# Kernel tuning notes

Measured on AMD Instinct MI355X. Metric: run time of the kernel, lower is better.

## Reference

```python
import jax, jax.numpy as jnp
import numpy as np

SCALE = 0.125  # 1/sqrt(D_head=64)
NEG_INF = -1.0e9


def setup_inputs() -> dict:
    key = jax.random.key(0)
    kq, kk, kv, km = jax.random.split(key, 4)
    B, L, N, D = 2, 2048, 16, 64
    query = jax.random.normal(kq, (B, L, N, D), dtype=jnp.float32)
    k = jax.random.normal(kk, (B, L, N, D), dtype=jnp.float32)
    v = jax.random.normal(kv, (B, L, N, D), dtype=jnp.float32)
    attn_mask = jax.random.randint(km, (B, L, L), 0, 2).astype(jnp.bool_)
    return {"query": query, "key": k, "value": v, "attn_mask": attn_mask}


def reference(query, key, value, attn_mask):
    # scores: [B, L_q, L_k, N]
    attention = jnp.einsum('bind,bjnd->bijn', query, key) * SCALE
    # mask broadcast over heads; True positions are masked out
    attention = jnp.where(attn_mask[:, :, :, None], NEG_INF, attention)
    # softmax over the key axis (dim=2), dropout p=0.0 is identity
    attention = jax.nn.softmax(attention, axis=2)
    context = jnp.einsum('bijn,bjnd->bind', attention, value)
    return (context, attention)
```

## Files before the change

### kernel.cpp

```cpp
#include <hip/hip_runtime.h>
#include <hip/hip_bf16.h>

typedef unsigned short u16;
typedef unsigned char u8;
typedef __attribute__((ext_vector_type(8))) short bf16x8;
typedef __attribute__((ext_vector_type(4))) float f32x4;

#define MFMA16(a, b, c) __builtin_amdgcn_mfma_f32_16x16x32_bf16(a, b, c, 0, 0, 0)

#define LGKM_BARRIER()                                     \
    do {                                                   \
        asm volatile("s_waitcnt lgkmcnt(0)" ::: "memory"); \
        __builtin_amdgcn_s_barrier();                      \
        asm volatile("" ::: "memory");                     \
    } while (0)

static __device__ __forceinline__ u16 f2bf(float f) {
    __hip_bfloat16 h = __float2bfloat16(f);
    return *reinterpret_cast<u16*>(&h);
}
static __device__ __forceinline__ float bf2f(u16 h) {
    unsigned u = ((unsigned)h) << 16;
    return __uint_as_float(u);
}

__global__ __launch_bounds__(256) void kconv_kernel(const float* __restrict__ kf,
                                                    u16* __restrict__ kb) {
    const size_t i = ((size_t)blockIdx.x * 256 + threadIdx.x) * 4;
    float4 f = *(const float4*)(kf + i);
    alignas(8) u16 w[4] = {f2bf(f.x), f2bf(f.y), f2bf(f.z), f2bf(f.w)};
    *(uint2*)(kb + i) = *(const uint2*)w;
}

__global__ __launch_bounds__(256) void vt_kernel(const float* __restrict__ v,
                                                 u16* __restrict__ vt) {
    __shared__ u16 T[64][72];
    const int t = threadIdx.x, bid = blockIdx.x;
    const int b = bid >> 9, n = bid & 15, j0 = ((bid >> 4) & 31) << 6;
    {
        const int jj = t >> 4, tt = t & 15;
#pragma unroll
        for (int rep = 0; rep < 4; rep++) {
            const int j = rep * 16 + jj;
            const float* src = v + (((size_t)((b * 2048 + j0 + j) * 16 + n)) << 6) + tt * 4;
            float4 f = *(const float4*)src;
            alignas(8) u16 w[4] = {f2bf(f.x), f2bf(f.y), f2bf(f.z), f2bf(f.w)};
            *(uint2*)&T[j][tt * 4] = *(const uint2*)w;
        }
    }
    __syncthreads();
    {
        const int d = t >> 2, jq = t & 3;
        alignas(16) u16 w[16];
#pragma unroll
        for (int e = 0; e < 16; e++) w[e] = T[jq * 16 + e][d];
        u16* dst = vt + (((size_t)((b * 16 + n) * 64 + d)) << 11) + j0 + jq * 16;
        *(uint4*)dst = *(const uint4*)&w[0];
        *(uint4*)(dst + 8) = *(const uint4*)&w[8];
    }
}

#define LOADK(ra, rb, rc2, rd, jb)                            \
    do {                                                      \
        const int jw_ = (jb) & 2047;                          \
        const u16* kp0_ = kb + (size_t)(jw_ + c) * 1024;      \
        ra = *(const bf16x8*)kp0_;                            \
        rb = *(const bf16x8*)(kp0_ + 32);                     \
        const u16* kp1_ = kb + (size_t)(jw_ + 16 + c) * 1024; \
        rc2 = *(const bf16x8*)kp1_;                           \
        rd = *(const bf16x8*)(kp1_ + 32);                     \
    } while (0)

#define LOADV(r0, r1, r2, r3, jb)                             \
    do {                                                      \
        const int jw_ = (jb) & 2047;                          \
        const u16* vp_ = vb + (size_t)c * 2048 + jw_ + g * 8; \
        r0 = *(const bf16x8*)(vp_);                           \
        r1 = *(const bf16x8*)(vp_ + 16 * 2048);               \
        r2 = *(const bf16x8*)(vp_ + 32 * 2048);               \
        r3 = *(const bf16x8*)(vp_ + 48 * 2048);               \
    } while (0)

__global__ __launch_bounds__(1024, 4) void attn_kernel(
    const float* __restrict__ qf, const u16* __restrict__ kb_g,
    const u16* __restrict__ vt, const void* __restrict__ mask,
    float* __restrict__ ctx, float* __restrict__ attn) {
    __shared__ u16 maskT[2048];
    __shared__ u16 pbuf[2][16][16][40];

    const int tid = threadIdx.x;
    const int lane = tid & 63;
    const int wv = tid >> 6;
    const int g = lane >> 4, c = lane & 15;
    const int rbit = g * 4;

    const int bid = blockIdx.x;
    const int b = ((bid & 7) < 4) ? 0 : 1;
    const int idx = ((bid >> 3) << 2) | (bid & 3);
    const int i0 = idx << 4;

    bool mask_is_u8;
    {
        unsigned acc = 0;
        const unsigned* mw = (const unsigned*)mask;
#pragma unroll
        for (int i = 0; i < 64; i++) acc |= mw[i];
        mask_is_u8 = (acc & 0xFFFFFF00u) != 0u;
    }

    {
        const size_t base = ((size_t)(b * 2048 + i0)) * 2048 + (size_t)tid * 2;
        unsigned m0 = 0, m1 = 0;
        if (mask_is_u8) {
            const u8* m8 = (const u8*)mask;
#pragma unroll
            for (int i = 0; i < 16; i++) {
                const u8* mp = m8 + base + (size_t)i * 2048;
                if (mp[0]) m0 |= (1u << i);
                if (mp[1]) m1 |= (1u << i);
            }
        } else {
            const int* m32 = (const int*)mask;
#pragma unroll
            for (int i = 0; i < 16; i++) {
                const int* mp = m32 + base + (size_t)i * 2048;
                if (mp[0]) m0 |= (1u << i);
                if (mp[1]) m1 |= (1u << i);
            }
        }
        *reinterpret_cast<unsigned*>(&maskT[tid * 2]) = m0 | (m1 << 16);
    }
    __syncthreads();

    bf16x8 aq0, aq1;
    {
        const float* qp = qf + (((size_t)(b * 2048 + i0 + c) * 16 + wv) << 6) + g * 8;
        float4 f0 = *(const float4*)qp;
        float4 f1 = *(const float4*)(qp + 4);
        float4 f2 = *(const float4*)(qp + 32);
        float4 f3 = *(const float4*)(qp + 36);
        alignas(16) u16 w0[8] = {f2bf(f0.x), f2bf(f0.y), f2bf(f0.z), f2bf(f0.w),
                                 f2bf(f1.x), f2bf(f1.y), f2bf(f1.z), f2bf(f1.w)};
        alignas(16) u16 w1[8] = {f2bf(f2.x), f2bf(f2.y), f2bf(f2.z), f2bf(f2.w),
                                 f2bf(f3.x), f2bf(f3.y), f2bf(f3.z), f2bf(f3.w)};
        aq0 = *(const bf16x8*)w0;
        aq1 = *(const bf16x8*)w1;
    }

    const u16* kb = kb_g + (((size_t)(b * 2048) * 16 + wv) << 6) + g * 8;
    const u16* vb = vt + (((size_t)(b * 16 + wv)) << 17);

    float l0 = 0.f, l1 = 0.f, l2 = 0.f, l3 = 0.f;
    bf16x8 pa0, pa1, pb0, pb1;
    {
        const u16* kp = kb + (size_t)c * 1024;
        pa0 = *(const bf16x8*)kp;
        pa1 = *(const bf16x8*)(kp + 32);
        const u16* kq = kb + (size_t)(16 + c) * 1024;
        pb0 = *(const bf16x8*)kq;
        pb1 = *(const bf16x8*)(kq + 32);
    }
    for (int j0 = 0; j0 < 2048; j0 += 32) {
        {
            f32x4 s = {0.f, 0.f, 0.f, 0.f};
            s = MFMA16(aq0, pa0, s);
            s = MFMA16(aq1, pa1, s);
            const int jw = (j0 + 32) & 2047;
            const u16* kp = kb + (size_t)(jw + c) * 1024;
            pa0 = *(const bf16x8*)kp;
            pa1 = *(const bf16x8*)(kp + 32);
            const unsigned mt = maskT[j0 + c];
            l0 += __expf(((mt >> (rbit + 0)) & 1) ? -1e9f : s[0] * 0.125f);
            l1 += __expf(((mt >> (rbit + 1)) & 1) ? -1e9f : s[1] * 0.125f);
            l2 += __expf(((mt >> (rbit + 2)) & 1) ? -1e9f : s[2] * 0.125f);
            l3 += __expf(((mt >> (rbit + 3)) & 1) ? -1e9f : s[3] * 0.125f);
        }
        {
            f32x4 s = {0.f, 0.f, 0.f, 0.f};
            s = MFMA16(aq0, pb0, s);
            s = MFMA16(aq1, pb1, s);
            const int jw = (j0 + 48) & 2047;
            const u16* kq = kb + (size_t)(jw + c) * 1024;
            pb0 = *(const bf16x8*)kq;
            pb1 = *(const bf16x8*)(kq + 32);
            const unsigned mt = maskT[j0 + 16 + c];
            l0 += __expf(((mt >> (rbit + 0)) & 1) ? -1e9f : s[0] * 0.125f);
            l1 += __expf(((mt >> (rbit + 1)) & 1) ? -1e9f : s[1] * 0.125f);
            l2 += __expf(((mt >> (rbit + 2)) & 1) ? -1e9f : s[2] * 0.125f);
            l3 += __expf(((mt >> (rbit + 3)) & 1) ? -1e9f : s[3] * 0.125f);
        }
    }
#pragma unroll
    for (int off = 1; off <= 8; off <<= 1) {
        l0 += __shfl_xor(l0, off);
        l1 += __shfl_xor(l1, off);
        l2 += __shfl_xor(l2, off);
        l3 += __shfl_xor(l3, off);
    }
    const float n0i = (l0 != 0.f) ? 1.f / l0 : 0.f;
    const float n1i = (l1 != 0.f) ? 1.f / l1 : 0.f;
    const float n2i = (l2 != 0.f) ? 1.f / l2 : 0.f;
    const float n3i = (l3 != 0.f) ? 1.f / l3 : 0.f;

    f32x4 o0 = {0.f, 0.f, 0.f, 0.f}, o1 = o0, o2 = o0, o3 = o0;

    const int wo_i = tid >> 6;
    const int wo_c = tid & 63;
    const int wo_j = wo_c >> 1;
    const int wo_n = (wo_c & 1) << 3;
    float* attn_row = attn + (((size_t)(b * 2048 + i0 + wo_i)) << 15) + wo_n;

#define HALF(pp, KA, KB, KC, KD, Va, Vb, Vc, Vd, jcur)                                 \
    do {                                                                               \
        {                                                                              \
            f32x4 s = {0.f, 0.f, 0.f, 0.f};                                            \
            s = MFMA16(aq0, KA, s);                                                    \
            s = MFMA16(aq1, KB, s);                                                    \
            const unsigned mt = maskT[(jcur) + c];                                     \
            pbuf[pp][wv][rbit + 0][c] =                                                \
                f2bf(__expf(((mt >> (rbit + 0)) & 1) ? -1e9f : s[0] * 0.125f) * n0i);  \
            pbuf[pp][wv][rbit + 1][c] =                                                \
                f2bf(__expf(((mt >> (rbit + 1)) & 1) ? -1e9f : s[1] * 0.125f) * n1i);  \
            pbuf[pp][wv][rbit + 2][c] =                                                \
                f2bf(__expf(((mt >> (rbit + 2)) & 1) ? -1e9f : s[2] * 0.125f) * n2i);  \
            pbuf[pp][wv][rbit + 3][c] =                                                \
                f2bf(__expf(((mt >> (rbit + 3)) & 1) ? -1e9f : s[3] * 0.125f) * n3i);  \
        }                                                                              \
        {                                                                              \
            f32x4 s = {0.f, 0.f, 0.f, 0.f};                                            \
            s = MFMA16(aq0, KC, s);                                                    \
            s = MFMA16(aq1, KD, s);                                                    \
            const unsigned mt = maskT[(jcur) + 16 + c];                                \
            pbuf[pp][wv][rbit + 0][16 + c] =                                           \
                f2bf(__expf(((mt >> (rbit + 0)) & 1) ? -1e9f : s[0] * 0.125f) * n0i);  \
            pbuf[pp][wv][rbit + 1][16 + c] =                                           \
                f2bf(__expf(((mt >> (rbit + 1)) & 1) ? -1e9f : s[1] * 0.125f) * n1i);  \
            pbuf[pp][wv][rbit + 2][16 + c] =                                           \
                f2bf(__expf(((mt >> (rbit + 2)) & 1) ? -1e9f : s[2] * 0.125f) * n2i);  \
            pbuf[pp][wv][rbit + 3][16 + c] =                                           \
                f2bf(__expf(((mt >> (rbit + 3)) & 1) ? -1e9f : s[3] * 0.125f) * n3i);  \
        }                                                                              \
        LOADK(KA, KB, KC, KD, (jcur) + 64);                                            \
        LGKM_BARRIER();                                                                \
        {                                                                              \
            const bf16x8 ap_ = *(const bf16x8*)&pbuf[pp][wv][c][g * 8];                \
            o0 = MFMA16(ap_, Va, o0);                                                  \
            o1 = MFMA16(ap_, Vb, o1);                                                  \
            o2 = MFMA16(ap_, Vc, o2);                                                  \
            o3 = MFMA16(ap_, Vd, o3);                                                  \
        }                                                                              \
        LOADV(Va, Vb, Vc, Vd, (jcur) + 64);                                            \
        __builtin_amdgcn_sched_barrier(0);                                             \
        {                                                                              \
            alignas(16) float w[8];                                                    \
            _Pragma("unroll") for (int e = 0; e < 8; e++)                              \
                w[e] = bf2f(pbuf[pp][wo_n + e][wo_i][wo_j]);                           \
            float* dst = attn_row + (size_t)((jcur) + wo_j) * 16;                      \
            *(f32x4*)dst = *(const f32x4*)&w[0];                                       \
            *(f32x4*)(dst + 4) = *(const f32x4*)&w[4];                                 \
        }                                                                              \
    } while (0)

    bf16x8 K0a, K0b, K0c, K0d, V00, V01, V02, V03;
    bf16x8 K1a, K1b, K1c, K1d, V10, V11, V12, V13;
    LOADK(K0a, K0b, K0c, K0d, 0);
    LOADV(V00, V01, V02, V03, 0);
    LOADK(K1a, K1b, K1c, K1d, 32);
    LOADV(V10, V11, V12, V13, 32);

    for (int j0 = 0; j0 < 2048; j0 += 64) {
        HALF(0, K0a, K0b, K0c, K0d, V00, V01, V02, V03, j0);
        HALF(1, K1a, K1b, K1c, K1d, V10, V11, V12, V13, j0 + 32);
    }
#undef HALF

#pragma unroll
    for (int r = 0; r < 4; r++) {
        float* cp = ctx + (((size_t)(b * 2048 + i0 + rbit + r) * 16 + wv) << 6) + c;
        cp[0]  = o0[r];
        cp[16] = o1[r];
        cp[32] = o2[r];
        cp[48] = o3[r];
    }
}

extern "C" void kernel_launch(void* const* d_in, const int* in_sizes, int n_in,
                              void* d_out, int out_size, void* d_ws, size_t ws_size,
                              hipStream_t stream) {
    const float* q   = (const float*)d_in[0];
    const float* k   = (const float*)d_in[1];
    const float* v   = (const float*)d_in[2];
    const void* mask = (const void*)d_in[3];

    float* ctx  = (float*)d_out;
    float* attn = (float*)d_out + 4194304;

    u16* vt = (u16*)d_ws;
    u16* kb = vt + 4194304;

    kconv_kernel<<<4096, 256, 0, stream>>>(k, kb);
    vt_kernel<<<1024, 256, 0, stream>>>(v, vt);
    attn_kernel<<<256, 1024, 0, stream>>>(q, kb, vt, mask, ctx, attn);
}
```

Measured before the change: 1.024 ms.

## Split heads across two 512-thread blocks per query tile

Each 16-row query tile is now handled by two 512-thread blocks, each owning eight heads, in place of one 1024-thread block covering all sixteen heads. The grid doubles to 512 blocks, and the block-to-tile mapping gains a head-half bit. The aim is more blocks in flight, finer scheduling and cheaper per-block barriers. The cost is that each block loads and transposes the mask tile on its own, so mask reads double, and the attention-row writes become half-row segments of eight heads.

```diff
diff --git a/kernel.cpp b/kernel.cpp
--- a/kernel.cpp
+++ b/kernel.cpp
@@ -81,23 +81,26 @@
         r3 = *(const bf16x8*)(vp_ + 48 * 2048);               \
     } while (0)
 
-__global__ __launch_bounds__(1024, 4) void attn_kernel(
+__global__ __launch_bounds__(512, 4) void attn_kernel(
     const float* __restrict__ qf, const u16* __restrict__ kb_g,
     const u16* __restrict__ vt, const void* __restrict__ mask,
     float* __restrict__ ctx, float* __restrict__ attn) {
     __shared__ u16 maskT[2048];
-    __shared__ u16 pbuf[2][16][16][40];
+    __shared__ u16 pbuf[2][8][16][40];
 
     const int tid = threadIdx.x;
     const int lane = tid & 63;
-    const int wv = tid >> 6;
+    const int wvl = tid >> 6;
     const int g = lane >> 4, c = lane & 15;
     const int rbit = g * 4;
 
     const int bid = blockIdx.x;
-    const int b = ((bid & 7) < 4) ? 0 : 1;
-    const int idx = ((bid >> 3) << 2) | (bid & 3);
-    const int i0 = idx << 4;
+    const int xcd = bid & 7;
+    const int b = (xcd < 4) ? 0 : 1;
+    const int hh = (bid >> 3) & 1;
+    const int i_tile = ((bid >> 4) << 2) | (bid & 3);
+    const int i0 = i_tile << 4;
+    const int wv = hh * 8 + wvl;
 
     bool mask_is_u8;
     {
@@ -109,8 +112,8 @@
     }
 
     {
-        const size_t base = ((size_t)(b * 2048 + i0)) * 2048 + (size_t)tid * 2;
-        unsigned m0 = 0, m1 = 0;
+        const size_t base = ((size_t)(b * 2048 + i0)) * 2048 + (size_t)tid * 4;
+        unsigned m0 = 0, m1 = 0, m2 = 0, m3 = 0;
         if (mask_is_u8) {
             const u8* m8 = (const u8*)mask;
 #pragma unroll
@@ -118,6 +121,8 @@
                 const u8* mp = m8 + base + (size_t)i * 2048;
                 if (mp[0]) m0 |= (1u << i);
                 if (mp[1]) m1 |= (1u << i);
+                if (mp[2]) m2 |= (1u << i);
+                if (mp[3]) m3 |= (1u << i);
             }
         } else {
             const int* m32 = (const int*)mask;
@@ -126,9 +131,14 @@
                 const int* mp = m32 + base + (size_t)i * 2048;
                 if (mp[0]) m0 |= (1u << i);
                 if (mp[1]) m1 |= (1u << i);
+                if (mp[2]) m2 |= (1u << i);
+                if (mp[3]) m3 |= (1u << i);
             }
         }
-        *reinterpret_cast<unsigned*>(&maskT[tid * 2]) = m0 | (m1 << 16);
+        uint2 packed;
+        packed.x = m0 | (m1 << 16);
+        packed.y = m2 | (m3 << 16);
+        *reinterpret_cast<uint2*>(&maskT[tid * 4]) = packed;
     }
     __syncthreads();
 
@@ -204,11 +214,9 @@
 
     f32x4 o0 = {0.f, 0.f, 0.f, 0.f}, o1 = o0, o2 = o0, o3 = o0;
 
-    const int wo_i = tid >> 6;
-    const int wo_c = tid & 63;
-    const int wo_j = wo_c >> 1;
-    const int wo_n = (wo_c & 1) << 3;
-    float* attn_row = attn + (((size_t)(b * 2048 + i0 + wo_i)) << 15) + wo_n;
+    const int wo_i = tid >> 5;
+    const int wo_j = tid & 31;
+    float* attn_row = attn + (((size_t)(b * 2048 + i0 + wo_i)) << 15) + hh * 8;
 
 #define HALF(pp, KA, KB, KC, KD, Va, Vb, Vc, Vd, jcur)                                 \
     do {                                                                               \
@@ -217,13 +225,13 @@
             s = MFMA16(aq0, KA, s);                                                    \
             s = MFMA16(aq1, KB, s);                                                    \
             const unsigned mt = maskT[(jcur) + c];                                     \
-            pbuf[pp][wv][rbit + 0][c] =                                                \
+            pbuf[pp][wvl][rbit + 0][c] =                                               \
                 f2bf(__expf(((mt >> (rbit + 0)) & 1) ? -1e9f : s[0] * 0.125f) * n0i);  \
-            pbuf[pp][wv][rbit + 1][c] =                                                \
+            pbuf[pp][wvl][rbit + 1][c] =                                               \
                 f2bf(__expf(((mt >> (rbit + 1)) & 1) ? -1e9f : s[1] * 0.125f) * n1i);  \
-            pbuf[pp][wv][rbit + 2][c] =                                                \
+            pbuf[pp][wvl][rbit + 2][c] =                                               \
                 f2bf(__expf(((mt >> (rbit + 2)) & 1) ? -1e9f : s[2] * 0.125f) * n2i);  \
-            pbuf[pp][wv][rbit + 3][c] =                                                \
+            pbuf[pp][wvl][rbit + 3][c] =                                               \
                 f2bf(__expf(((mt >> (rbit + 3)) & 1) ? -1e9f : s[3] * 0.125f) * n3i);  \
         }                                                                              \
         {                                                                              \
@@ -231,19 +239,19 @@
             s = MFMA16(aq0, KC, s);                                                    \
             s = MFMA16(aq1, KD, s);                                                    \
             const unsigned mt = maskT[(jcur) + 16 + c];                                \
-            pbuf[pp][wv][rbit + 0][16 + c] =                                           \
+            pbuf[pp][wvl][rbit + 0][16 + c] =                                          \
                 f2bf(__expf(((mt >> (rbit + 0)) & 1) ? -1e9f : s[0] * 0.125f) * n0i);  \
-            pbuf[pp][wv][rbit + 1][16 + c] =                                           \
+            pbuf[pp][wvl][rbit + 1][16 + c] =                                          \
                 f2bf(__expf(((mt >> (rbit + 1)) & 1) ? -1e9f : s[1] * 0.125f) * n1i);  \
-            pbuf[pp][wv][rbit + 2][16 + c] =                                           \
+            pbuf[pp][wvl][rbit + 2][16 + c] =                                          \
                 f2bf(__expf(((mt >> (rbit + 2)) & 1) ? -1e9f : s[2] * 0.125f) * n2i);  \
-            pbuf[pp][wv][rbit + 3][16 + c] =                                           \
+            pbuf[pp][wvl][rbit + 3][16 + c] =                                          \
                 f2bf(__expf(((mt >> (rbit + 3)) & 1) ? -1e9f : s[3] * 0.125f) * n3i);  \
         }                                                                              \
         LOADK(KA, KB, KC, KD, (jcur) + 64);                                            \
         LGKM_BARRIER();                                                                \
         {                                                                              \
-            const bf16x8 ap_ = *(const bf16x8*)&pbuf[pp][wv][c][g * 8];                \
+            const bf16x8 ap_ = *(const bf16x8*)&pbuf[pp][wvl][c][g * 8];               \
             o0 = MFMA16(ap_, Va, o0);                                                  \
             o1 = MFMA16(ap_, Vb, o1);                                                  \
             o2 = MFMA16(ap_, Vc, o2);                                                  \
@@ -254,7 +262,7 @@
         {                                                                              \
             alignas(16) float w[8];                                                    \
             _Pragma("unroll") for (int e = 0; e < 8; e++)                              \
-                w[e] = bf2f(pbuf[pp][wo_n + e][wo_i][wo_j]);                           \
+                w[e] = bf2f(pbuf[pp][e][wo_i][wo_j]);                                  \
             float* dst = attn_row + (size_t)((jcur) + wo_j) * 16;                      \
             *(f32x4*)dst = *(const f32x4*)&w[0];                                       \
             *(f32x4*)(dst + 4) = *(const f32x4*)&w[4];                                 \
@@ -300,5 +308,5 @@
 
     kconv_kernel<<<4096, 256, 0, stream>>>(k, kb);
     vt_kernel<<<1024, 256, 0, stream>>>(v, vt);
-    attn_kernel<<<256, 1024, 0, stream>>>(q, kb, vt, mask, ctx, attn);
-}
+    attn_kernel<<<512, 512, 0, stream>>>(q, kb, vt, mask, ctx, attn);
+}
```

After: 1.064 ms. +3.9%, slower.
